# Performance work log

Hardware: AMD Instinct MI355X
Metric: run time of the kernel (lower is better)

## Reference

```python
import jax, jax.numpy as jnp
import numpy as np

N, E, XD, H, L, G, C = 20000, 320000, 128, 256, 4, 128, 10
EPS = 1e-5


def setup_inputs() -> dict:
    key = jax.random.key(0)
    ks = jax.random.split(key, 24)
    s = 0.05
    inp = {
        "x": jax.random.normal(ks[0], (N, XD), jnp.float32),
        "edge_index": jax.random.randint(ks[1], (2, E), 0, N, jnp.int32),
        "batch": jnp.sort(jax.random.randint(ks[2], (N,), 0, G, jnp.int32)),
        "encW": jax.random.normal(ks[3], (XD, H), jnp.float32) * s,
        "encB": jnp.zeros((H,), jnp.float32),
        "convW": jax.random.normal(ks[4], (L, H, H), jnp.float32) * s,
        "convB": jnp.zeros((L, H), jnp.float32),
        "bnG": jnp.ones((L, H), jnp.float32),
        "bnB": jnp.zeros((L, H), jnp.float32),
        "fcW1": jax.random.normal(ks[5], (H, H), jnp.float32) * s,
        "fcB1": jnp.zeros((H,), jnp.float32),
        "fcG1": jnp.ones((H,), jnp.float32),
        "fcBe1": jnp.zeros((H,), jnp.float32),
        "fcW2": jax.random.normal(ks[6], (H, H), jnp.float32) * s,
        "fcB2": jnp.zeros((H,), jnp.float32),
        "fcG2": jnp.ones((H,), jnp.float32),
        "fcBe2": jnp.zeros((H,), jnp.float32),
        "fcW3": jax.random.normal(ks[7], (H, C), jnp.float32) * s,
        "fcB3": jnp.zeros((C,), jnp.float32),
    }
    return inp


def _bn(h, g, b):
    # BatchNorm1d, training-mode batch statistics (biased var), eps=1e-5
    m = h.mean(0)
    v = h.var(0)
    return g * (h - m) * jax.lax.rsqrt(v + EPS) + b


def _forward(x, edge_index, batch, encW, encB, convW, convB, bnG, bnB,
             fcW1, fcB1, fcG1, fcBe1, fcW2, fcB2, fcG2, fcBe2, fcW3, fcB3):
    src, dst = edge_index[0], edge_index[1]
    # GCN symmetric normalization with implicit self-loops (fill value 1)
    deg = jax.ops.segment_sum(jnp.ones((E,), x.dtype), dst, num_segments=N) + 1.0
    dinv = jax.lax.rsqrt(deg)
    enorm = (dinv[src] * dinv[dst])[:, None]       # [E,1]
    self_norm = (dinv * dinv)[:, None]             # [N,1] self-loop coeff

    h = x @ encW + encB                            # node encoder
    for i in range(L):
        t = h @ convW[i]                           # GCNConv linear (no bias)
        agg = jax.ops.segment_sum(t[src] * enorm, dst, num_segments=N)
        t = agg + t * self_norm + convB[i]         # aggregate + self loop + bias
        h = jax.nn.relu(_bn(t, bnG[i], bnB[i]))    # dropout is identity (eval)

    # global mean pool over graph ids
    sums = jax.ops.segment_sum(h, batch, num_segments=G)
    cnts = jax.ops.segment_sum(jnp.ones((N,), h.dtype), batch, num_segments=G)
    g = sums / jnp.maximum(cnts, 1.0)[:, None]     # [G,H]

    # fc_out: MLP(Linear->BN->ReLU->Linear) -> BN -> Linear
    m = jax.nn.relu(_bn(g @ fcW1 + fcB1, fcG1, fcBe1)) @ fcW2 + fcB2
    m = _bn(m, fcG2, fcBe2)
    return m @ fcW3 + fcB3                         # [G,C]


def reference(x, edge_index, batch, encW, encB, convW, convB, bnG, bnB,
              fcW1, fcB1, fcG1, fcBe1, fcW2, fcB2, fcG2, fcBe2, fcW3, fcB3):
    return _forward(x, edge_index, batch, encW, encB, convW, convB, bnG, bnB,
                    fcW1, fcB1, fcG1, fcBe1, fcW2, fcB2, fcG2, fcBe2, fcW3, fcB3)
```

## Files before the change

kernel.cpp:

```cpp
#include <hip/hip_runtime.h>
#include <hip/hip_bf16.h>
#include <cstddef>

#define N_NODES 20000
#define N_EDGES 320000
#define XDIM 128
#define H 256
#define LAYERS 4
#define G_GRAPHS 128
#define C_OUT 10
#define EPS_BN 1e-5f
#define NSLOT 64
#define NB 8

typedef __attribute__((ext_vector_type(8))) short short8;
typedef __attribute__((ext_vector_type(4))) float f32x4;
typedef __attribute__((address_space(3))) unsigned int lds_u32;
typedef const __attribute__((address_space(1))) unsigned int glob_u32;

__global__ void hist_kernel(const int* __restrict__ dst, int* __restrict__ cnt, int E) {
    int e = blockIdx.x * blockDim.x + threadIdx.x;
    if (e < E) atomicAdd(&cnt[dst[e]], 1);
}

__global__ void scan_kernel(const int* __restrict__ cnt, int* __restrict__ rowstart,
                            float* __restrict__ dinv, int N) {
    __shared__ int partial[1024];
    int tid = threadIdx.x;
    int chunk = (N + 1023) / 1024;
    int start = tid * chunk;
    int lsum = 0;
    for (int i = 0; i < chunk; ++i) {
        int idx = start + i;
        if (idx < N) {
            int c = cnt[idx];
            dinv[idx] = 1.0f / sqrtf((float)c + 1.0f);
            lsum += c;
        }
    }
    partial[tid] = lsum;
    __syncthreads();
    for (int off = 1; off < 1024; off <<= 1) {
        int v = (tid >= off) ? partial[tid - off] : 0;
        __syncthreads();
        partial[tid] += v;
        __syncthreads();
    }
    int run = (tid == 0) ? 0 : partial[tid - 1];
    for (int i = 0; i < chunk; ++i) {
        int idx = start + i;
        if (idx < N) { rowstart[idx] = run; run += cnt[idx]; }
    }
    if (tid == 1023) rowstart[N] = partial[1023];
}

__global__ void fill_kernel(const int* __restrict__ src, const int* __restrict__ dst,
                            const int* __restrict__ rowstart, int* __restrict__ cursor,
                            const float* __restrict__ dinv,
                            int* __restrict__ csr_src, float* __restrict__ csr_w, int E) {
    int e = blockIdx.x * blockDim.x + threadIdx.x;
    if (e < E) {
        int s = src[e], d = dst[e];
        int pos = rowstart[d] + atomicAdd(&cursor[d], 1);
        csr_src[pos] = s;
        csr_w[pos] = dinv[s] * dinv[d];
    }
}

__global__ void prep_kernel(const float* __restrict__ x, const float* __restrict__ encW,
                            const float* __restrict__ convW,
                            __hip_bfloat16* __restrict__ xbf,
                            __hip_bfloat16* __restrict__ encWT,
                            __hip_bfloat16* __restrict__ convWT) {
    int i = blockIdx.x * blockDim.x + threadIdx.x;
    const int nx = N_NODES * XDIM;
    const int ne = XDIM * H;
    const int nc = LAYERS * H * H;
    if (i < nx) {
        xbf[i] = __float2bfloat16(x[i]);
    } else if (i < nx + ne) {
        int j = i - nx;
        int r = j / H, c = j - r * H;
        encWT[c * XDIM + r] = __float2bfloat16(encW[j]);
    } else if (i < nx + ne + nc) {
        int j = i - nx - ne;
        int l = j / (H * H), rem = j - l * (H * H);
        int r = rem / H, c = rem - r * H;
        convWT[(size_t)l * H * H + c * H + r] = __float2bfloat16(convW[j]);
    }
}

__device__ __forceinline__ short bf16bits(float x) {
    __hip_bfloat16 b = __float2bfloat16(x);
    return *(short*)&b;
}

template <int K, bool FUSE_BN>
__global__ __launch_bounds__(256) void gemm_bf16_kernel(
    const void* __restrict__ Ain,
    const __hip_bfloat16* __restrict__ BT,
    const float* __restrict__ bias,
    const float* __restrict__ spart,
    const float* __restrict__ gamma,
    const float* __restrict__ beta,
    __hip_bfloat16* __restrict__ Cbf,
    int M, int Nn) {
    __shared__ short As[2][64 * 32];
    __shared__ short Bs[2][128 * 32];
    __shared__ float scs[H];
    __shared__ float shs[H];
    const short* Ash = (const short*)Ain;
    const float* Af = (const float*)Ain;
    const short* Bsh = (const short*)BT;
    int tid = threadIdx.x;
    int lane = tid & 63;
    int wave = tid >> 6;
    int quad = lane >> 4;
    int lr = lane & 15;
    int wm = (wave & 1) * 32;
    int wn = (wave >> 1) * 64;
    int Mblk = blockIdx.x * 64;
    int Nblk = blockIdx.y * 128;

    f32x4 acc[2][4];
#pragma unroll
    for (int i = 0; i < 2; ++i)
#pragma unroll
        for (int j = 0; j < 4; ++j) acc[i][j] = (f32x4){0.f, 0.f, 0.f, 0.f};

    int srow = tid >> 2, sqs = tid & 3;
    int sqg = sqs ^ ((srow >> 1) & 3);
    int arow = Mblk + srow; if (arow >= M) arow = M - 1;
    int s1 = 256 + tid;
    int brow0 = Nblk + (tid >> 2);
    int qg0 = sqg;
    int brow1 = Nblk + (s1 >> 2);
    int qg1 = (s1 & 3) ^ (((s1 >> 2) >> 1) & 3);

    if (FUSE_BN) {
        int c = tid;
        float s = 0.f, s2 = 0.f;
#pragma unroll 8
        for (int i = 0; i < NSLOT; ++i) {
            s  += spart[(size_t)i * (2 * H) + c];
            s2 += spart[(size_t)i * (2 * H) + H + c];
        }
        float invN = 1.0f / (float)N_NODES;
        float mean = s * invN;
        float var = s2 * invN - mean * mean;
        float kk = gamma[c] / sqrtf(var + EPS_BN);
        scs[c] = kk;
        shs[c] = beta[c] - mean * kk;
        __syncthreads();
    }

    float4 ra0, ra1;
    auto loadA_f = [&](int k0) {
        int kc = k0 + sqg * 8;
        ra0 = *(const float4*)(Af + (size_t)arow * K + kc);
        ra1 = *(const float4*)(Af + (size_t)arow * K + kc + 4);
    };
    auto storeA_f = [&](int buf, int k0) {
        int kc = k0 + sqg * 8;
        float4 c0 = *(const float4*)&scs[kc];
        float4 c1 = *(const float4*)&scs[kc + 4];
        float4 h0 = *(const float4*)&shs[kc];
        float4 h1 = *(const float4*)&shs[kc + 4];
        short8 pk;
        pk[0] = bf16bits(fmaxf(ra0.x * c0.x + h0.x, 0.f));
        pk[1] = bf16bits(fmaxf(ra0.y * c0.y + h0.y, 0.f));
        pk[2] = bf16bits(fmaxf(ra0.z * c0.z + h0.z, 0.f));
        pk[3] = bf16bits(fmaxf(ra0.w * c0.w + h0.w, 0.f));
        pk[4] = bf16bits(fmaxf(ra1.x * c1.x + h1.x, 0.f));
        pk[5] = bf16bits(fmaxf(ra1.y * c1.y + h1.y, 0.f));
        pk[6] = bf16bits(fmaxf(ra1.z * c1.z + h1.z, 0.f));
        pk[7] = bf16bits(fmaxf(ra1.w * c1.w + h1.w, 0.f));
        *(short8*)&As[buf][srow * 32 + sqs * 8] = pk;
    };
    auto stageA_async = [&](int buf, int k0) {
        __builtin_amdgcn_global_load_lds((glob_u32*)(Ash + (size_t)arow * K + k0 + sqg * 8),
                                         (lds_u32*)&As[buf][0] + wave * 256, 16, 0, 0);
    };
    auto stageB = [&](int buf, int k0) {
        __builtin_amdgcn_global_load_lds((glob_u32*)(Bsh + (size_t)brow0 * K + k0 + qg0 * 8),
                                         (lds_u32*)&Bs[buf][0] + wave * 256, 16, 0, 0);
        __builtin_amdgcn_global_load_lds((glob_u32*)(Bsh + (size_t)brow1 * K + k0 + qg1 * 8),
                                         (lds_u32*)&Bs[buf][0] + 1024 + wave * 256, 16, 0, 0);
    };

    constexpr int NK = K / 32;
    if (FUSE_BN) loadA_f(0); else stageA_async(0, 0);
    stageB(0, 0);
#pragma unroll
    for (int k = 0; k < NK; ++k) {
        int buf = k & 1;
        if (FUSE_BN) storeA_f(buf, k * 32);
        __syncthreads();
        if (k + 1 < NK) {
            if (FUSE_BN) loadA_f((k + 1) * 32); else stageA_async(buf ^ 1, (k + 1) * 32);
            stageB(buf ^ 1, (k + 1) * 32);
        }
        short8 af[2], bfr[4];
#pragma unroll
        for (int mi = 0; mi < 2; ++mi) {
            int r = wm + mi * 16 + lr;
            af[mi] = *(const short8*)&As[buf][r * 32 + (quad ^ ((r >> 1) & 3)) * 8];
        }
#pragma unroll
        for (int ni = 0; ni < 4; ++ni) {
            int r = wn + ni * 16 + lr;
            bfr[ni] = *(const short8*)&Bs[buf][r * 32 + (quad ^ ((r >> 1) & 3)) * 8];
        }
#pragma unroll
        for (int mi = 0; mi < 2; ++mi)
#pragma unroll
            for (int ni = 0; ni < 4; ++ni)
                acc[mi][ni] = __builtin_amdgcn_mfma_f32_16x16x32_bf16(af[mi], bfr[ni], acc[mi][ni], 0, 0, 0);
    }
#pragma unroll
    for (int mi = 0; mi < 2; ++mi) {
#pragma unroll
        for (int r = 0; r < 4; ++r) {
            int m = Mblk + wm + mi * 16 + quad * 4 + r;
            if (m < M) {
#pragma unroll
                for (int ni = 0; ni < 4; ++ni) {
                    int n = Nblk + wn + ni * 16 + lr;
                    float v = acc[mi][ni][r];
                    if (bias) v += bias[n];
                    Cbf[(size_t)m * Nn + n] = __float2bfloat16(v);
                }
            }
        }
    }
}

__global__ __launch_bounds__(256) void agg_kernel(const __hip_bfloat16* __restrict__ t,
                           const int* __restrict__ rowstart,
                           const int* __restrict__ csr_src,
                           const float* __restrict__ csr_w,
                           const float* __restrict__ dinv,
                           const float* __restrict__ convB,
                           float* __restrict__ out,
                           float* __restrict__ spart,
                           int N) {
    __shared__ float red[4][256];
    int tid = threadIdx.x;
    int wave = tid >> 6;
    int lane = tid & 63;
    int sub = lane >> 5;
    int hl = lane & 31;
    int stream = wave * 2 + sub;
    int c0 = hl * 8;
    const ushort* tp = (const ushort*)t;
    float sv = 0.f, sq = 0.f;
    int n0 = blockIdx.x * NB;
#pragma unroll 1
    for (int it = 0; it < NB; ++it) {
        int n = n0 + it;
        int s = rowstart[n], e = rowstart[n + 1];
        float a[8] = {};
#pragma unroll 1
        for (int j0 = s; j0 < e; j0 += 16) {
#pragma unroll
            for (int u = 0; u < 2; ++u) {
                int j = j0 + u * 8 + stream;
                int idx = n; float w = 0.f;
                if (j < e) { idx = csr_src[j]; w = csr_w[j]; }
                uint4 v = *(const uint4*)(tp + (size_t)idx * H + c0);
                a[0] += __uint_as_float(v.x << 16) * w;
                a[1] += __uint_as_float(v.x & 0xffff0000u) * w;
                a[2] += __uint_as_float(v.y << 16) * w;
                a[3] += __uint_as_float(v.y & 0xffff0000u) * w;
                a[4] += __uint_as_float(v.z << 16) * w;
                a[5] += __uint_as_float(v.z & 0xffff0000u) * w;
                a[6] += __uint_as_float(v.w << 16) * w;
                a[7] += __uint_as_float(v.w & 0xffff0000u) * w;
            }
        }
#pragma unroll
        for (int k = 0; k < 8; ++k) a[k] += __shfl_xor(a[k], 32);
        if (sub == 0) {
            *(float4*)&red[wave][c0] = make_float4(a[0], a[1], a[2], a[3]);
            *(float4*)&red[wave][c0 + 4] = make_float4(a[4], a[5], a[6], a[7]);
        }
        __syncthreads();
        int c = tid;
        float val = red[0][c] + red[1][c] + red[2][c] + red[3][c];
        float dn = dinv[n];
        val += __bfloat162float(t[(size_t)n * H + c]) * (dn * dn) + convB[c];
        out[(size_t)n * H + c] = val;
        sv += val; sq += val * val;
        __syncthreads();
    }
    float* sp = spart + (size_t)(blockIdx.x & (NSLOT - 1)) * (2 * H);
    atomicAdd(&sp[tid], sv);
    atomicAdd(&sp[H + tid], sq);
}

__global__ __launch_bounds__(256) void pool_kernel(const float* __restrict__ t2,
                            const int* __restrict__ batch,
                            const float* __restrict__ spart,
                            const float* __restrict__ gamma,
                            const float* __restrict__ beta,
                            float* __restrict__ g, int N) {
    __shared__ float4 red[4][64];
    __shared__ float scs[H];
    __shared__ float shs[H];
    {
        int c = threadIdx.x;
        float s = 0.f, s2 = 0.f;
#pragma unroll 8
        for (int i = 0; i < NSLOT; ++i) {
            s  += spart[(size_t)i * (2 * H) + c];
            s2 += spart[(size_t)i * (2 * H) + H + c];
        }
        float invN = 1.0f / (float)N_NODES;
        float mean = s * invN;
        float var = s2 * invN - mean * mean;
        float kk = gamma[c] / sqrtf(var + EPS_BN);
        scs[c] = kk;
        shs[c] = beta[c] - mean * kk;
    }
    __syncthreads();
    int gid = blockIdx.x;
    int lo = 0, hi = N;
    while (lo < hi) { int mid = (lo + hi) >> 1; if (batch[mid] < gid) lo = mid + 1; else hi = mid; }
    int s = lo;
    lo = s; hi = N;
    while (lo < hi) { int mid = (lo + hi) >> 1; if (batch[mid] < gid + 1) lo = mid + 1; else hi = mid; }
    int e = lo;
    int wave = threadIdx.x >> 6;
    int lane = threadIdx.x & 63;
    float4 scv = *(const float4*)&scs[lane * 4];
    float4 shv = *(const float4*)&shs[lane * 4];
    float a0 = 0.f, a1 = 0.f, a2 = 0.f, a3 = 0.f;
    for (int r = s + wave; r < e; r += 4) {
        float4 v = *(const float4*)(t2 + (size_t)r * H + lane * 4);
        a0 += __bfloat162float(__float2bfloat16(fmaxf(v.x * scv.x + shv.x, 0.f)));
        a1 += __bfloat162float(__float2bfloat16(fmaxf(v.y * scv.y + shv.y, 0.f)));
        a2 += __bfloat162float(__float2bfloat16(fmaxf(v.z * scv.z + shv.z, 0.f)));
        a3 += __bfloat162float(__float2bfloat16(fmaxf(v.w * scv.w + shv.w, 0.f)));
    }
    red[wave][lane] = make_float4(a0, a1, a2, a3);
    __syncthreads();
    int c = threadIdx.x;
    const float* rf = (const float*)red;
    float sum = rf[c] + rf[256 + c] + rf[512 + c] + rf[768 + c];
    g[(size_t)gid * H + c] = sum / fmaxf((float)(e - s), 1.0f);
}

template <int K, int NN>
__global__ __launch_bounds__(256) void fc_lds_kernel(const float* __restrict__ in,
                                                     const float* __restrict__ W,
                                                     const float* __restrict__ b,
                                                     float* __restrict__ out) {
    __shared__ float row[K];
    int g = blockIdx.x;
    for (int k = threadIdx.x; k < K; k += 256) row[k] = in[(size_t)g * K + k];
    __syncthreads();
    int hc = threadIdx.x;
    if (hc < NN) {
        float acc = b[hc];
#pragma unroll
        for (int k = 0; k < K; ++k) acc += row[k] * W[k * NN + hc];
        out[(size_t)g * NN + hc] = acc;
    }
}

__global__ void fc_out_kernel(const float* __restrict__ in, const float* __restrict__ W,
                              const float* __restrict__ b, float* __restrict__ out) {
    int t = blockIdx.x * blockDim.x + threadIdx.x;
    if (t >= G_GRAPHS * C_OUT) return;
    int g = t / C_OUT, c = t % C_OUT;
    float acc = b[c];
#pragma unroll 16
    for (int k = 0; k < H; ++k) acc += in[(size_t)g * H + k] * W[k * C_OUT + c];
    out[t] = acc;
}

__global__ void bn_head_kernel(const float* __restrict__ in, const float* __restrict__ gamma,
                               const float* __restrict__ beta, float* __restrict__ out,
                               int Grows, int relu) {
    int c = blockIdx.x;
    int r = threadIdx.x;
    __shared__ float red[G_GRAPHS];
    float v = in[r * H + c];
    red[r] = v;
    __syncthreads();
    for (int off = G_GRAPHS / 2; off > 0; off >>= 1) {
        if (r < off) red[r] += red[r + off];
        __syncthreads();
    }
    float mean = red[0] / (float)Grows;
    __syncthreads();
    float d = v - mean;
    red[r] = d * d;
    __syncthreads();
    for (int off = G_GRAPHS / 2; off > 0; off >>= 1) {
        if (r < off) red[r] += red[r + off];
        __syncthreads();
    }
    float var = red[0] / (float)Grows;
    float y = gamma[c] * d / sqrtf(var + EPS_BN) + beta[c];
    if (relu) y = fmaxf(y, 0.f);
    out[r * H + c] = y;
}

extern "C" void kernel_launch(void* const* d_in, const int* in_sizes, int n_in,
                              void* d_out, int out_size, void* d_ws, size_t ws_size,
                              hipStream_t stream) {
    const float* x     = (const float*)d_in[0];
    const int*   edge  = (const int*)d_in[1];
    const int*   batch = (const int*)d_in[2];
    const float* encW  = (const float*)d_in[3];
    const float* encB  = (const float*)d_in[4];
    const float* convW = (const float*)d_in[5];
    const float* convB = (const float*)d_in[6];
    const float* bnG   = (const float*)d_in[7];
    const float* bnB   = (const float*)d_in[8];
    const float* fcW1  = (const float*)d_in[9];
    const float* fcB1  = (const float*)d_in[10];
    const float* fcG1  = (const float*)d_in[11];
    const float* fcBe1 = (const float*)d_in[12];
    const float* fcW2  = (const float*)d_in[13];
    const float* fcB2  = (const float*)d_in[14];
    const float* fcG2  = (const float*)d_in[15];
    const float* fcBe2 = (const float*)d_in[16];
    const float* fcW3  = (const float*)d_in[17];
    const float* fcB3  = (const float*)d_in[18];
    float* out = (float*)d_out;

    const int* srcIdx = edge;
    const int* dstIdx = edge + N_EDGES;

    char* base = (char*)d_ws;
    size_t off = 0;
    auto alloc = [&](size_t bytes) -> void* {
        void* p = base + off;
        off = (off + bytes + 255) & ~(size_t)255;
        return p;
    };
    int*   cnt      = (int*)alloc(N_NODES * 4);
    int*   cursor   = (int*)alloc(N_NODES * 4);
    int*   rowstart = (int*)alloc((N_NODES + 1) * 4);
    float* dinv     = (float*)alloc(N_NODES * 4);
    int*   csr_src  = (int*)alloc(N_EDGES * 4);
    float* csr_w    = (float*)alloc(N_EDGES * 4);
    float* spart    = (float*)alloc((size_t)LAYERS * NSLOT * 2 * H * 4);
    __hip_bfloat16* xbf    = (__hip_bfloat16*)alloc((size_t)N_NODES * XDIM * 2);
    __hip_bfloat16* encWT  = (__hip_bfloat16*)alloc((size_t)H * XDIM * 2);
    __hip_bfloat16* convWT = (__hip_bfloat16*)alloc((size_t)LAYERS * H * H * 2);
    __hip_bfloat16* hbf    = (__hip_bfloat16*)alloc((size_t)N_NODES * H * 2);
    __hip_bfloat16* tbf    = (__hip_bfloat16*)alloc((size_t)N_NODES * H * 2);
    float* t2buf = (float*)alloc((size_t)N_NODES * H * 4);
    float* gpool = (float*)alloc(G_GRAPHS * H * 4);
    float* m1    = (float*)alloc(G_GRAPHS * H * 4);
    float* m2    = (float*)alloc(G_GRAPHS * H * 4);

    hipMemsetAsync(cnt, 0, (size_t)((char*)rowstart - (char*)cnt), stream);
    hipMemsetAsync(spart, 0, (size_t)LAYERS * NSLOT * 2 * H * 4, stream);

    hist_kernel<<<(N_EDGES + 255) / 256, 256, 0, stream>>>(dstIdx, cnt, N_EDGES);
    scan_kernel<<<1, 1024, 0, stream>>>(cnt, rowstart, dinv, N_NODES);
    fill_kernel<<<(N_EDGES + 255) / 256, 256, 0, stream>>>(srcIdx, dstIdx, rowstart, cursor,
                                                           dinv, csr_src, csr_w, N_EDGES);

    {
        int total = N_NODES * XDIM + XDIM * H + LAYERS * H * H;
        prep_kernel<<<(total + 255) / 256, 256, 0, stream>>>(x, encW, convW, xbf, encWT, convWT);
    }

    dim3 gridG((N_NODES + 63) / 64, H / 128);
    gemm_bf16_kernel<XDIM, false><<<gridG, 256, 0, stream>>>(
        xbf, encWT, encB, nullptr, nullptr, nullptr, hbf, N_NODES, H);

    for (int l = 0; l < LAYERS; ++l) {
        float* spartL = spart + (size_t)l * NSLOT * 2 * H;
        if (l == 0) {
            gemm_bf16_kernel<H, false><<<gridG, 256, 0, stream>>>(
                hbf, convWT + (size_t)l * H * H, nullptr, nullptr, nullptr, nullptr,
                tbf, N_NODES, H);
        } else {
            float* spartP = spart + (size_t)(l - 1) * NSLOT * 2 * H;
            gemm_bf16_kernel<H, true><<<gridG, 256, 0, stream>>>(
                t2buf, convWT + (size_t)l * H * H, nullptr,
                spartP, bnG + (size_t)(l - 1) * H, bnB + (size_t)(l - 1) * H,
                tbf, N_NODES, H);
        }
        agg_kernel<<<N_NODES / NB, 256, 0, stream>>>(tbf, rowstart, csr_src, csr_w, dinv,
                                                     convB + l * H, t2buf, spartL, N_NODES);
    }

    pool_kernel<<<G_GRAPHS, 256, 0, stream>>>(
        t2buf, batch, spart + (size_t)(LAYERS - 1) * NSLOT * 2 * H,
        bnG + (size_t)(LAYERS - 1) * H, bnB + (size_t)(LAYERS - 1) * H, gpool, N_NODES);

    fc_lds_kernel<H, H><<<G_GRAPHS, 256, 0, stream>>>(gpool, fcW1, fcB1, m1);
    bn_head_kernel<<<H, G_GRAPHS, 0, stream>>>(m1, fcG1, fcBe1, m1, G_GRAPHS, 1);
    fc_lds_kernel<H, H><<<G_GRAPHS, 256, 0, stream>>>(m1, fcW2, fcB2, m2);
    bn_head_kernel<<<H, G_GRAPHS, 0, stream>>>(m2, fcG2, fcBe2, m2, G_GRAPHS, 0);
    fc_out_kernel<<<(G_GRAPHS * C_OUT + 255) / 256, 256, 0, stream>>>(m2, fcW3, fcB3, out);
}
```

Before: 446.6 us.

## Restructure GCN aggregation to per-wave nodes with column-quarter blocks, no LDS sync

The aggregation kernel no longer has a whole block cooperate on each node with LDS reduction and two barriers. Each wave now owns 8 nodes, and each block covers a quarter of the 256 feature columns. Lanes split edges four ways and reduce with cross-lane shuffles. This removes the __syncthreads and LDS traffic and lets waves progress independently. In exchange, each gathered row read is only 8 bytes per lane, the src/weight indices are re-read by four blocks, and there are more atomics to the stats slots.

```diff
diff --git a/kernel.cpp b/kernel.cpp
--- a/kernel.cpp
+++ b/kernel.cpp
@@ -11,7 +11,7 @@
 #define C_OUT 10
 #define EPS_BN 1e-5f
 #define NSLOT 64
-#define NB 8
+#define NPW 8
 
 typedef __attribute__((ext_vector_type(8))) short short8;
 typedef __attribute__((ext_vector_type(4))) float f32x4;
@@ -244,58 +244,62 @@
                            float* __restrict__ out,
                            float* __restrict__ spart,
                            int N) {
-    __shared__ float red[4][256];
     int tid = threadIdx.x;
     int wave = tid >> 6;
     int lane = tid & 63;
-    int sub = lane >> 5;
-    int hl = lane & 31;
-    int stream = wave * 2 + sub;
-    int c0 = hl * 8;
+    int q = blockIdx.x & 3;
+    int grp = blockIdx.x >> 2;
+    int es = lane >> 4;
+    int cl = lane & 15;
+    int cbase = q * 64 + cl * 4;
     const ushort* tp = (const ushort*)t;
-    float sv = 0.f, sq = 0.f;
-    int n0 = blockIdx.x * NB;
+    float b0 = convB[cbase], b1 = convB[cbase + 1], b2 = convB[cbase + 2], b3 = convB[cbase + 3];
+    float sv0 = 0.f, sv1 = 0.f, sv2 = 0.f, sv3 = 0.f;
+    float sq0 = 0.f, sq1 = 0.f, sq2 = 0.f, sq3 = 0.f;
 #pragma unroll 1
-    for (int it = 0; it < NB; ++it) {
-        int n = n0 + it;
+    for (int it = 0; it < NPW; ++it) {
+        int n = grp * (4 * NPW) + wave * NPW + it;
         int s = rowstart[n], e = rowstart[n + 1];
-        float a[8] = {};
-#pragma unroll 1
-        for (int j0 = s; j0 < e; j0 += 16) {
-#pragma unroll
-            for (int u = 0; u < 2; ++u) {
-                int j = j0 + u * 8 + stream;
-                int idx = n; float w = 0.f;
-                if (j < e) { idx = csr_src[j]; w = csr_w[j]; }
-                uint4 v = *(const uint4*)(tp + (size_t)idx * H + c0);
-                a[0] += __uint_as_float(v.x << 16) * w;
-                a[1] += __uint_as_float(v.x & 0xffff0000u) * w;
-                a[2] += __uint_as_float(v.y << 16) * w;
-                a[3] += __uint_as_float(v.y & 0xffff0000u) * w;
-                a[4] += __uint_as_float(v.z << 16) * w;
-                a[5] += __uint_as_float(v.z & 0xffff0000u) * w;
-                a[6] += __uint_as_float(v.w << 16) * w;
-                a[7] += __uint_as_float(v.w & 0xffff0000u) * w;
-            }
-        }
-#pragma unroll
-        for (int k = 0; k < 8; ++k) a[k] += __shfl_xor(a[k], 32);
-        if (sub == 0) {
-            *(float4*)&red[wave][c0] = make_float4(a[0], a[1], a[2], a[3]);
-            *(float4*)&red[wave][c0 + 4] = make_float4(a[4], a[5], a[6], a[7]);
-        }
-        __syncthreads();
-        int c = tid;
-        float val = red[0][c] + red[1][c] + red[2][c] + red[3][c];
+        float a0 = 0.f, a1 = 0.f, a2 = 0.f, a3 = 0.f;
+        for (int j = s + es; j < e; j += 4) {
+            int idx = csr_src[j];
+            float w = csr_w[j];
+            uint2 v = *(const uint2*)(tp + (size_t)idx * H + cbase);
+            a0 += __uint_as_float(v.x << 16) * w;
+            a1 += __uint_as_float(v.x & 0xffff0000u) * w;
+            a2 += __uint_as_float(v.y << 16) * w;
+            a3 += __uint_as_float(v.y & 0xffff0000u) * w;
+        }
+        a0 += __shfl_xor(a0, 16); a0 += __shfl_xor(a0, 32);
+        a1 += __shfl_xor(a1, 16); a1 += __shfl_xor(a1, 32);
+        a2 += __shfl_xor(a2, 16); a2 += __shfl_xor(a2, 32);
+        a3 += __shfl_xor(a3, 16); a3 += __shfl_xor(a3, 32);
         float dn = dinv[n];
-        val += __bfloat162float(t[(size_t)n * H + c]) * (dn * dn) + convB[c];
-        out[(size_t)n * H + c] = val;
-        sv += val; sq += val * val;
-        __syncthreads();
-    }
-    float* sp = spart + (size_t)(blockIdx.x & (NSLOT - 1)) * (2 * H);
-    atomicAdd(&sp[tid], sv);
-    atomicAdd(&sp[H + tid], sq);
+        float ws = dn * dn;
+        uint2 vs = *(const uint2*)(tp + (size_t)n * H + cbase);
+        a0 += __uint_as_float(vs.x << 16) * ws + b0;
+        a1 += __uint_as_float(vs.x & 0xffff0000u) * ws + b1;
+        a2 += __uint_as_float(vs.y << 16) * ws + b2;
+        a3 += __uint_as_float(vs.y & 0xffff0000u) * ws + b3;
+        if (es == 0) {
+            *(float4*)(out + (size_t)n * H + cbase) = make_float4(a0, a1, a2, a3);
+            sv0 += a0; sq0 += a0 * a0;
+            sv1 += a1; sq1 += a1 * a1;
+            sv2 += a2; sq2 += a2 * a2;
+            sv3 += a3; sq3 += a3 * a3;
+        }
+    }
+    if (es == 0) {
+        float* sp = spart + (size_t)((blockIdx.x * 4 + wave) & (NSLOT - 1)) * (2 * H);
+        atomicAdd(&sp[cbase], sv0);
+        atomicAdd(&sp[cbase + 1], sv1);
+        atomicAdd(&sp[cbase + 2], sv2);
+        atomicAdd(&sp[cbase + 3], sv3);
+        atomicAdd(&sp[H + cbase], sq0);
+        atomicAdd(&sp[H + cbase + 1], sq1);
+        atomicAdd(&sp[H + cbase + 2], sq2);
+        atomicAdd(&sp[H + cbase + 3], sq3);
+    }
 }
 
 __global__ __launch_bounds__(256) void pool_kernel(const float* __restrict__ t2,
@@ -475,6 +479,7 @@
     gemm_bf16_kernel<XDIM, false><<<gridG, 256, 0, stream>>>(
         xbf, encWT, encB, nullptr, nullptr, nullptr, hbf, N_NODES, H);
 
+    int aggBlocks = (N_NODES / (4 * NPW)) * 4;
     for (int l = 0; l < LAYERS; ++l) {
         float* spartL = spart + (size_t)l * NSLOT * 2 * H;
         if (l == 0) {
@@ -488,8 +493,8 @@
                 spartP, bnG + (size_t)(l - 1) * H, bnB + (size_t)(l - 1) * H,
                 tbf, N_NODES, H);
         }
-        agg_kernel<<<N_NODES / NB, 256, 0, stream>>>(tbf, rowstart, csr_src, csr_w, dinv,
-                                                     convB + l * H, t2buf, spartL, N_NODES);
+        agg_kernel<<<aggBlocks, 256, 0, stream>>>(tbf, rowstart, csr_src, csr_w, dinv,
+                                                  convB + l * H, t2buf, spartL, N_NODES);
     }
 
     pool_kernel<<<G_GRAPHS, 256, 0, stream>>>(
```

After: 583.7 us. 1.31x slower.
